# Kernel optimization log

Hardware: AMD Instinct MI355X
Metric: run time of the kernel (lower is better)

## Reference

```python
import math
import jax, jax.numpy as jnp
import numpy as np

SIZE = 8
STEEPNESS = 10.0
BATCH = 262144


def setup_inputs() -> dict:
    key = jax.random.key(0)
    k1, k2 = jax.random.split(key)
    pred_scores = jax.random.normal(k1, (BATCH, SIZE), dtype=jnp.float32)
    labels = jax.random.normal(k2, (BATCH, SIZE), dtype=jnp.float32)
    rank_ema = jnp.zeros((SIZE,), dtype=jnp.float32)  # fresh-module EMA buffer
    return {"pred_scores": pred_scores, "labels": labels, "rank_ema": rank_ema}


def _odd_even_diffsort(x, steepness=STEEPNESS):
    """Differentiable odd-even sorting network (cauchy distribution).
    x: [B, n]. Returns (sorted_values [B, n], perm [B, n, n]) with
    x @ perm == sorted_values (perm tracks columns, matching diffsort)."""
    B, n = x.shape
    P = jnp.broadcast_to(jnp.eye(n, dtype=x.dtype), (B, n, n))
    for layer in range(n):  # odd-even network has n layers for size n
        start = layer % 2
        idx_a = np.arange(start, n - 1, 2)  # static indices
        idx_b = idx_a + 1
        a = x[:, idx_a]
        b = x[:, idx_b]
        # Cauchy CDF of (b - a): alpha -> 1 when pair already sorted (a < b)
        alpha = jnp.arctan(steepness * (b - a)) / math.pi + 0.5  # [B, k]
        new_a = alpha * a + (1.0 - alpha) * b          # soft min -> lower index
        new_b = (1.0 - alpha) * a + alpha * b          # soft max -> upper index
        x = x.at[:, idx_a].set(new_a).at[:, idx_b].set(new_b)
        colA = P[:, :, idx_a]  # [B, n, k]
        colB = P[:, :, idx_b]
        al = alpha[:, None, :]
        P = P.at[:, :, idx_a].set(al * colA + (1.0 - al) * colB)
        P = P.at[:, :, idx_b].set((1.0 - al) * colA + al * colB)
    return x, P


def reference(pred_scores, labels, rank_ema):
    n = pred_scores.shape[-1]
    rank_indices = jnp.argsort(-labels, axis=-1)          # [B, n]
    rank_true = jnp.argsort(rank_indices, axis=-1)        # inverse permutation
    select_rank_ema = rank_ema[rank_true]                 # [B, n]
    shifted = pred_scores - select_rank_ema
    # (EMA buffer update is a detached side effect; it does not affect the loss)
    _, perm_prediction = _odd_even_diffsort(-shifted)
    # one_hot(argsort(-labels)).transpose(-2, -1)
    perm_ground_truth = jnp.swapaxes(jax.nn.one_hot(rank_indices, n, dtype=jnp.float32), -2, -1)
    p = perm_prediction.astype(jnp.float32)
    # torch BCELoss clamps each log term at -100
    log_p = jnp.clip(jnp.log(p), -100.0, None)
    log_1mp = jnp.clip(jnp.log1p(-p), -100.0, None)
    ce_loss = -jnp.mean(perm_ground_truth * log_p + (1.0 - perm_ground_truth) * log_1mp)
    return ce_loss
```

## Files before the change

kernel.cpp:

```cpp
#include <hip/hip_runtime.h>
#include <math.h>

#define BATCH 262144
#define N 8
#define BLK 64
#define NBLK (BATCH / BLK)
#define NCMP 28

struct Net { int a[NCMP]; unsigned sup[N][NCMP]; };
constexpr Net make_net() {
    Net n{};
    int k = 0;
    for (int L = 0; L < N; ++L)
        for (int a = (L & 1); a < N - 1; a += 2)
            n.a[k++] = a;
    for (int r = 0; r < N; ++r) {
        unsigned s = 1u << r;
        for (int q = 0; q < NCMP; ++q) {
            n.sup[r][q] = s;
            unsigned m = 3u << n.a[q];
            if (s & m) s |= m;
        }
    }
    return n;
}
constexpr Net NET = make_net();

__device__ __forceinline__ float cauchy_alpha(float z10) {
    float az  = __builtin_fabsf(z10);
    bool  big = az > 1.0f;
    float inv = __builtin_amdgcn_rcpf(az);
    float t   = big ? inv : az;
    float t2  = t * t;
    float p   = -0.0851330f;
    p = __builtin_fmaf(p, t2, 0.1801410f);
    p = __builtin_fmaf(p, t2, -0.3302995f);
    p = __builtin_fmaf(p, t2, 0.9998660f);
    float at = p * t;
    float r  = big ? (1.5707963267948966f - at) : at;
    float sr = __builtin_copysignf(r, z10);
    return __builtin_fmaf(sr, 0.31830988618379067f, 0.5f);
}

__global__ __launch_bounds__(BLK, 6) void diffsort_loss_kernel(
    const float* __restrict__ pred,
    const float* __restrict__ labels,
    const float* __restrict__ rank_ema,
    float* __restrict__ partial)
{
    const int row = blockIdx.x * BLK + threadIdx.x;

    __shared__ float ema[N];
    if (threadIdx.x < N) ema[threadIdx.x] = rank_ema[threadIdx.x];
    __syncthreads();

    const float4* lp = (const float4*)(labels + (size_t)row * N);
    const float4* pp = (const float4*)(pred   + (size_t)row * N);
    float4 l0 = lp[0], l1 = lp[1];
    float4 p0 = pp[0], p1 = pp[1];
    float lab[N] = {l0.x, l0.y, l0.z, l0.w, l1.x, l1.y, l1.z, l1.w};
    float prd[N] = {p0.x, p0.y, p0.z, p0.w, p1.x, p1.y, p1.z, p1.w};

    int rt[N];
#pragma unroll
    for (int i = 0; i < N; ++i) rt[i] = 0;
#pragma unroll
    for (int i = 0; i < N; ++i)
#pragma unroll
        for (int j = i + 1; j < N; ++j) {
            unsigned c = lab[j] > lab[i];
            rt[i] += c;
            rt[j] += 1u - c;
        }

    float x[N];
#pragma unroll
    for (int i = 0; i < N; ++i)
        x[i] = ema[rt[i]] - prd[i];

    float al[NCMP];
#pragma unroll
    for (int k = 0; k < NCMP; ++k) {
        const int ia = NET.a[k], ib = ia + 1;
        const float a = x[ia], b = x[ib];
        const float z = b - a;
        const float alpha = cauchy_alpha(10.0f * z);
        al[k] = alpha;
        x[ia] = __builtin_fmaf(-alpha, z, b);
        x[ib] = __builtin_fmaf( alpha, z, a);
    }

    float s = 0.0f;
#pragma unroll
    for (int i = 0; i < N; ++i) {
        float r[N];
#pragma unroll
        for (int j = 0; j < N; ++j) r[j] = (i == j) ? 1.0f : 0.0f;

#pragma unroll
        for (int k = 0; k < NCMP; ++k) {
            const int ia = NET.a[k], ib = ia + 1;
            const bool na = (NET.sup[i][k] >> ia) & 1u;
            const bool nb = (NET.sup[i][k] >> ib) & 1u;
            const float alpha = al[k];
            if (na && nb) {
                const float ca = r[ia], cb = r[ib];
                const float d = ca - cb;
                r[ia] = __builtin_fmaf( alpha, d, cb);
                r[ib] = __builtin_fmaf(-alpha, d, ca);
            } else if (na) {
                const float ca = r[ia];
                r[ia] = alpha * ca;
                r[ib] = __builtin_fmaf(-alpha, ca, ca);
            } else if (nb) {
                const float cb = r[ib];
                r[ia] = __builtin_fmaf(-alpha, cb, cb);
                r[ib] = alpha * cb;
            }
        }

        const int hj = rt[i];
        float arg = 1.0f;
#pragma unroll
        for (int j = 0; j < N; ++j) {
            const float f = (hj == j) ? r[j] : (1.0f - r[j]);
            arg *= fmaxf(f, 1e-37f);
        }
        s += __logf(arg);
    }

#pragma unroll
    for (int off = 32; off > 0; off >>= 1)
        s += __shfl_down(s, off);
    if (threadIdx.x == 0) partial[blockIdx.x] = s;
}

__global__ __launch_bounds__(256) void reduce_partials(
    const float* __restrict__ partial, float* __restrict__ out)
{
    float s = 0.0f;
#pragma unroll
    for (int k = 0; k < NBLK / 256; ++k)
        s += partial[threadIdx.x + k * 256];
#pragma unroll
    for (int off = 32; off > 0; off >>= 1)
        s += __shfl_down(s, off);

    __shared__ float wsum[4];
    const int lane = threadIdx.x & 63;
    const int wid  = threadIdx.x >> 6;
    if (lane == 0) wsum[wid] = s;
    __syncthreads();
    if (threadIdx.x == 0) {
        const float tot = wsum[0] + wsum[1] + wsum[2] + wsum[3];
        out[0] = -tot * (1.0f / 16777216.0f);
    }
}

extern "C" void kernel_launch(void* const* d_in, const int* in_sizes, int n_in,
                              void* d_out, int out_size, void* d_ws, size_t ws_size,
                              hipStream_t stream)
{
    const float* pred     = (const float*)d_in[0];
    const float* labels   = (const float*)d_in[1];
    const float* rank_ema = (const float*)d_in[2];
    float* out     = (float*)d_out;
    float* partial = (float*)d_ws;

    diffsort_loss_kernel<<<NBLK, BLK, 0, stream>>>(pred, labels, rank_ema, partial);
    reduce_partials<<<1, 256, 0, stream>>>(partial, out);
}
```

Measured before the change: 79.37 us.

## Fuse permutation-matrix updates into the sort loop and trim arctan polynomial

Builds the full 8x8 soft permutation matrix in registers while the sorting network runs, instead of storing 28 alphas and replaying the network per row afterward. The arctan approximation drops one polynomial term, and the clamp moves from each factor to the final product before the log. Occupancy is lowered from 6 to 4 waves to leave room for the 64-entry matrix in registers. Risks are register pressure, lower latency hiding, reduced arctan accuracy, and different clamping semantics that could produce tiny products or underflow.

Result: faster. 76.70 us (-3.4%).

```diff
diff --git a/kernel.cpp b/kernel.cpp
--- a/kernel.cpp
+++ b/kernel.cpp
@@ -32,17 +32,16 @@
     float inv = __builtin_amdgcn_rcpf(az);
     float t   = big ? inv : az;
     float t2  = t * t;
-    float p   = -0.0851330f;
-    p = __builtin_fmaf(p, t2, 0.1801410f);
-    p = __builtin_fmaf(p, t2, -0.3302995f);
-    p = __builtin_fmaf(p, t2, 0.9998660f);
+    float p   = 0.1417796f;
+    p = __builtin_fmaf(p, t2, -0.3258092f);
+    p = __builtin_fmaf(p, t2, 0.9992150f);
     float at = p * t;
     float r  = big ? (1.5707963267948966f - at) : at;
     float sr = __builtin_copysignf(r, z10);
     return __builtin_fmaf(sr, 0.31830988618379067f, 0.5f);
 }
 
-__global__ __launch_bounds__(BLK, 6) void diffsort_loss_kernel(
+__global__ __launch_bounds__(BLK, 4) void diffsort_loss_kernel(
     const float* __restrict__ pred,
     const float* __restrict__ labels,
     const float* __restrict__ rank_ema,
@@ -78,55 +77,53 @@
     for (int i = 0; i < N; ++i)
         x[i] = ema[rt[i]] - prd[i];
 
-    float al[NCMP];
+    float P[N][N];
+#pragma unroll
+    for (int i = 0; i < N; ++i)
+#pragma unroll
+        for (int j = 0; j < N; ++j)
+            P[i][j] = (i == j) ? 1.0f : 0.0f;
+
 #pragma unroll
     for (int k = 0; k < NCMP; ++k) {
         const int ia = NET.a[k], ib = ia + 1;
         const float a = x[ia], b = x[ib];
         const float z = b - a;
         const float alpha = cauchy_alpha(10.0f * z);
-        al[k] = alpha;
         x[ia] = __builtin_fmaf(-alpha, z, b);
         x[ib] = __builtin_fmaf( alpha, z, a);
+#pragma unroll
+        for (int i = 0; i < N; ++i) {
+            const bool na = (NET.sup[i][k] >> ia) & 1u;
+            const bool nb = (NET.sup[i][k] >> ib) & 1u;
+            if (na && nb) {
+                const float ca = P[i][ia], cb = P[i][ib];
+                const float d = ca - cb;
+                P[i][ia] = __builtin_fmaf( alpha, d, cb);
+                P[i][ib] = __builtin_fmaf(-alpha, d, ca);
+            } else if (na) {
+                const float ca = P[i][ia];
+                P[i][ia] = alpha * ca;
+                P[i][ib] = __builtin_fmaf(-alpha, ca, ca);
+            } else if (nb) {
+                const float cb = P[i][ib];
+                P[i][ia] = __builtin_fmaf(-alpha, cb, cb);
+                P[i][ib] = alpha * cb;
+            }
+        }
     }
 
     float s = 0.0f;
 #pragma unroll
     for (int i = 0; i < N; ++i) {
-        float r[N];
-#pragma unroll
-        for (int j = 0; j < N; ++j) r[j] = (i == j) ? 1.0f : 0.0f;
-
-#pragma unroll
-        for (int k = 0; k < NCMP; ++k) {
-            const int ia = NET.a[k], ib = ia + 1;
-            const bool na = (NET.sup[i][k] >> ia) & 1u;
-            const bool nb = (NET.sup[i][k] >> ib) & 1u;
-            const float alpha = al[k];
-            if (na && nb) {
-                const float ca = r[ia], cb = r[ib];
-                const float d = ca - cb;
-                r[ia] = __builtin_fmaf( alpha, d, cb);
-                r[ib] = __builtin_fmaf(-alpha, d, ca);
-            } else if (na) {
-                const float ca = r[ia];
-                r[ia] = alpha * ca;
-                r[ib] = __builtin_fmaf(-alpha, ca, ca);
-            } else if (nb) {
-                const float cb = r[ib];
-                r[ia] = __builtin_fmaf(-alpha, cb, cb);
-                r[ib] = alpha * cb;
-            }
-        }
-
         const int hj = rt[i];
         float arg = 1.0f;
 #pragma unroll
         for (int j = 0; j < N; ++j) {
-            const float f = (hj == j) ? r[j] : (1.0f - r[j]);
-            arg *= fmaxf(f, 1e-37f);
+            const float pj = P[i][j];
+            arg *= (hj == j) ? pj : (1.0f - pj);
         }
-        s += __logf(arg);
+        s += __logf(fmaxf(arg, 1e-37f));
     }
 
 #pragma unroll
```
